# Kernel tuning notes

Measured on AMD Instinct MI355X. Metric: run time of the kernel, lower is better.

Reference implementation:

```python
import jax, jax.numpy as jnp
import numpy as np

N_NODES = 100000
N_EDGES = 1600000
IN_SIZE, HID_SIZE, OUT_SIZE = 128, 64, 64


def _glorot(key, shape):
    lim = float(np.sqrt(6.0 / (shape[0] + shape[1])))
    return jax.random.uniform(key, shape, jnp.float32, -lim, lim)


def setup_inputs() -> dict:
    key = jax.random.key(0)
    ks = jax.random.split(key, 6)
    features = jax.random.normal(ks[0], (N_NODES, IN_SIZE), jnp.float32)
    src = jax.random.randint(ks[1], (N_EDGES,), 0, N_NODES)
    dst = jax.random.randint(ks[2], (N_EDGES,), 0, N_NODES)
    return {
        "features": features,
        "W0": _glorot(ks[3], (IN_SIZE, HID_SIZE)),
        "b0": jnp.zeros((HID_SIZE,), jnp.float32),
        "W1": _glorot(ks[4], (HID_SIZE, HID_SIZE)),
        "b1": jnp.zeros((HID_SIZE,), jnp.float32),
        "W2": _glorot(ks[5], (HID_SIZE, OUT_SIZE)),
        "b2": jnp.zeros((OUT_SIZE,), jnp.float32),
        "src": src,
        "dst": dst,
    }


def reference(features, W0, b0, W1, b1, W2, b2, src, dst):
    # DGL GraphConv with norm='both': h' = relu(D_in^{-1/2} A D_out^{-1/2} h W + b)
    # Dropout layers are identity in eval mode (deterministic baseline).
    N = features.shape[0]
    ones = jnp.ones(src.shape, features.dtype)
    deg_out = jax.ops.segment_sum(ones, src, num_segments=N)
    deg_in = jax.ops.segment_sum(ones, dst, num_segments=N)
    norm_src = jnp.where(deg_out > 0, deg_out, 1.0) ** -0.5  # [N]
    norm_dst = jnp.where(deg_in > 0, deg_in, 1.0) ** -0.5    # [N]

    def layer(h, W, b):
        h = h * norm_src[:, None]          # source-side degree norm
        m = (h @ W)[src]                   # project first (in >= out), then gather [E, d_out]
        agg = jax.ops.segment_sum(m, dst, num_segments=N)  # scatter-add to destinations
        return jax.nn.relu(agg * norm_dst[:, None] + b)

    h = layer(features, W0, b0)
    h = layer(h, W1, b1)
    return layer(h, W2, b2)
```

## Files before the change

kernel.cpp:

```cpp
#include <hip/hip_runtime.h>
#include <hip/hip_bf16.h>

typedef __hip_bfloat16 bf16;
typedef __attribute__((ext_vector_type(8))) short bf16x8;
typedef __attribute__((ext_vector_type(8))) unsigned short u16x8;
typedef __attribute__((ext_vector_type(4))) float f32x4;
typedef __attribute__((ext_vector_type(4))) int i32x4;
typedef __attribute__((ext_vector_type(4))) short s16x4;

__device__ __forceinline__ float b2f(unsigned short u) {
  return __uint_as_float(((unsigned)u) << 16);
}
__device__ __forceinline__ unsigned short f2b(float x) {
  bf16 h = __float2bfloat16(x);
  return *reinterpret_cast<unsigned short*>(&h);
}

__global__ void k_passA(const int* __restrict__ src, const int* __restrict__ dst, int E,
                        int nbuck, int M, int* __restrict__ counts,
                        const unsigned short* __restrict__ raw, int* __restrict__ flag) {
  if (blockIdx.x == 256) {
    __shared__ int sbad, snz;
    const int t = threadIdx.x;
    if (t == 0) { sbad = 0; snz = 0; }
    __syncthreads();
    const unsigned short u = raw[t];
    const float a = fabsf(b2f(u));
    if (!(a < 100.f)) atomicAdd(&sbad, 1);
    if (((t & 1) == 0) && u != 0) atomicAdd(&snz, 1);
    __syncthreads();
    if (t == 0) flag[0] = (sbad == 0 && snz > 0) ? 1 : 0;
    return;
  }
  extern __shared__ int lh[];
  int* lh1 = lh;
  int* lh2 = lh + nbuck;
  const int t = threadIdx.x;
  for (int k = t; k < 2 * nbuck; k += 256) lh[k] = 0;
  __syncthreads();
  const int chunk = (E + 255) / 256;
  const int s = blockIdx.x * chunk;
  const int e = min(E, s + chunk);
  for (int i = s + t; i < e; i += 256) {
    atomicAdd(&lh1[dst[i] >> 8], 1);
    atomicAdd(&lh2[src[i] >> 8], 1);
  }
  __syncthreads();
  for (int k = t; k < nbuck; k += 256) {
    counts[k * 256 + blockIdx.x] = lh1[k];
    counts[M + k * 256 + blockIdx.x] = lh2[k];
  }
}

__global__ void k_scan1(const int* __restrict__ a, int M2, int* __restrict__ bsums) {
  __shared__ int sdata[256];
  int i = blockIdx.x * 256 + threadIdx.x;
  int v = (i < M2) ? a[i] : 0;
  sdata[threadIdx.x] = v;
  __syncthreads();
  for (int s = 128; s > 0; s >>= 1) {
    if (threadIdx.x < s) sdata[threadIdx.x] += sdata[threadIdx.x + s];
    __syncthreads();
  }
  if (threadIdx.x == 0) bsums[blockIdx.x] = sdata[0];
}

__global__ void k_scan2(int* __restrict__ bsums, int nb, int* __restrict__ rowStart,
                        int N, int E) {
  __shared__ int s[1024];
  const int t = threadIdx.x;
  const int v = (t < nb) ? bsums[t] : 0;
  s[t] = v;
  __syncthreads();
  for (int off = 1; off < 1024; off <<= 1) {
    int u = (t >= off) ? s[t - off] : 0;
    __syncthreads();
    s[t] += u;
    __syncthreads();
  }
  if (t < nb) bsums[t] = s[t] - v;
  if (t == 0) rowStart[N] = E;
}

__global__ void k_scan3(int* __restrict__ a, int M2, const int* __restrict__ bsums) {
  __shared__ int sdata[256];
  int i = blockIdx.x * 256 + threadIdx.x;
  int v = (i < M2) ? a[i] : 0;
  sdata[threadIdx.x] = v;
  __syncthreads();
  for (int off = 1; off < 256; off <<= 1) {
    int t = (threadIdx.x >= off) ? sdata[threadIdx.x - off] : 0;
    __syncthreads();
    sdata[threadIdx.x] += t;
    __syncthreads();
  }
  if (i < M2) a[i] = bsums[blockIdx.x] + sdata[threadIdx.x] - v;
}

__global__ void k_passC(const int* __restrict__ src, const int* __restrict__ dst, int E,
                        int nbuck, int M, const int* __restrict__ S,
                        int* __restrict__ tmp, unsigned char* __restrict__ tmp2) {
  extern __shared__ int cur[];
  int* cur1 = cur;
  int* cur2 = cur + nbuck;
  const int t = threadIdx.x;
  for (int k = t; k < nbuck; k += 256) {
    cur1[k] = S[k * 256 + blockIdx.x];
    cur2[k] = S[M + k * 256 + blockIdx.x];
  }
  __syncthreads();
  const int chunk = (E + 255) / 256;
  const int s = blockIdx.x * chunk;
  const int e = min(E, s + chunk);
  for (int i = s + t; i < e; i += 256) {
    const int sv = src[i];
    const int d = dst[i];
    const int pos1 = atomicAdd(&cur1[d >> 8], 1);
    tmp[pos1] = sv | ((d & 255) << 20);
    const int pos2 = atomicAdd(&cur2[sv >> 8], 1);
    tmp2[pos2 - E] = (unsigned char)(sv & 255);
  }
}

__global__ void k_passD(const int* __restrict__ tmp, const unsigned char* __restrict__ tmp2,
                        const int* __restrict__ S, int nbuck, int M, int N, int E,
                        int* __restrict__ rowStart, int* __restrict__ edgeSrc,
                        float* __restrict__ ns, float* __restrict__ nd) {
  __shared__ int h[256];
  __shared__ int ex[256];
  __shared__ int c[256];
  const int t = threadIdx.x;
  const int k = blockIdx.x;
  const int node = k * 256 + t;
  const int bs2 = S[M + k * 256] - E;
  const int be2 = (k + 1 < nbuck) ? (S[M + (k + 1) * 256] - E) : E;
  h[t] = 0;
  __syncthreads();
  for (int i = bs2 + t; i < be2; i += 256) atomicAdd(&h[tmp2[i]], 1);
  __syncthreads();
  if (node < N) {
    int dov = h[t];
    if (dov <= 0) dov = 1;
    ns[node] = rsqrtf((float)dov);
  }
  __syncthreads();
  const int bs = S[k * 256];
  const int be = (k + 1 < nbuck) ? S[(k + 1) * 256] : E;
  h[t] = 0;
  __syncthreads();
  for (int i = bs + t; i < be; i += 256) atomicAdd(&h[tmp[i] >> 20], 1);
  __syncthreads();
  const int cnt = h[t];
  ex[t] = cnt;
  __syncthreads();
  for (int off = 1; off < 256; off <<= 1) {
    int u = (t >= off) ? ex[t - off] : 0;
    __syncthreads();
    ex[t] += u;
    __syncthreads();
  }
  const int excl = ex[t] - cnt;
  if (node < N) {
    rowStart[node] = bs + excl;
    nd[node] = rsqrtf((float)(cnt > 0 ? cnt : 1));
  }
  c[t] = bs + excl;
  __syncthreads();
  for (int i = bs + t; i < be; i += 256) {
    const int v = tmp[i];
    const int pos = atomicAdd(&c[v >> 20], 1);
    edgeSrc[pos] = v & 0xFFFFF;
  }
}

template <int K, bool FIRST, bool SCALE>
__global__ void k_gemm(const void* __restrict__ hin, const void* __restrict__ Wv,
                       const int* __restrict__ flag, const float* __restrict__ norm_src,
                       int N, unsigned short* __restrict__ out) {
  const bool isb = (*flag != 0);
  const int lane = threadIdx.x & 63;
  const int quad = lane >> 4;
  const int l16 = lane & 15;
  constexpr int KT = K / 32;

  bf16x8 Bf[KT][4];
  {
    const unsigned short* Wus = (const unsigned short*)Wv;
    const float* Wf = (const float*)Wv;
#pragma unroll
    for (int kt = 0; kt < KT; ++kt)
#pragma unroll
      for (int nt = 0; nt < 4; ++nt)
#pragma unroll
        for (int j = 0; j < 8; ++j) {
          const int k = kt * 32 + quad * 8 + j;
          const int n = nt * 16 + l16;
          const float w = isb ? b2f(Wus[k * 64 + n]) : Wf[k * 64 + n];
          Bf[kt][nt][j] = (short)f2b(w);
        }
  }
  const int wid = (blockIdx.x * blockDim.x + threadIdx.x) >> 6;
  const int nw = (gridDim.x * blockDim.x) >> 6;
  const int G = (N + 15) >> 4;
  for (int g = wid; g < G; g += nw) {
    int rowA = (g << 4) + l16;
    if (rowA >= N) rowA = N - 1;
    f32x4 acc[4] = {{0.f, 0.f, 0.f, 0.f}, {0.f, 0.f, 0.f, 0.f},
                    {0.f, 0.f, 0.f, 0.f}, {0.f, 0.f, 0.f, 0.f}};
#pragma unroll
    for (int kt = 0; kt < KT; ++kt) {
      const int koff = kt * 32 + quad * 8;
      bf16x8 Af;
      if (FIRST && !isb) {
        const float* hp = (const float*)hin + (size_t)rowA * K + koff;
        const float4 u0 = *(const float4*)hp;
        const float4 u1 = *(const float4*)(hp + 4);
        Af[0] = (short)f2b(u0.x); Af[1] = (short)f2b(u0.y);
        Af[2] = (short)f2b(u0.z); Af[3] = (short)f2b(u0.w);
        Af[4] = (short)f2b(u1.x); Af[5] = (short)f2b(u1.y);
        Af[6] = (short)f2b(u1.z); Af[7] = (short)f2b(u1.w);
      } else {
        Af = *(const bf16x8*)((const unsigned short*)hin + (size_t)rowA * K + koff);
      }
      acc[0] = __builtin_amdgcn_mfma_f32_16x16x32_bf16(Af, Bf[kt][0], acc[0], 0, 0, 0);
      acc[1] = __builtin_amdgcn_mfma_f32_16x16x32_bf16(Af, Bf[kt][1], acc[1], 0, 0, 0);
      acc[2] = __builtin_amdgcn_mfma_f32_16x16x32_bf16(Af, Bf[kt][2], acc[2], 0, 0, 0);
      acc[3] = __builtin_amdgcn_mfma_f32_16x16x32_bf16(Af, Bf[kt][3], acc[3], 0, 0, 0);
    }
    const int rowD = (g << 4) + quad * 4;
#pragma unroll
    for (int r = 0; r < 4; ++r) {
      if (rowD + r < N) {
        const float f = SCALE ? norm_src[rowD + r] : 1.0f;
        const size_t o = (size_t)(rowD + r) * 64 + l16;
#pragma unroll
        for (int nt = 0; nt < 4; ++nt)
          out[o + nt * 16] = f2b(SCALE ? acc[nt][r] * f : acc[nt][r]);
      }
    }
  }
}

__device__ __forceinline__ void agg_chunk_compute(unsigned trbase, int cb32, int lo,
                                                  unsigned span, int quad, f32x4* acc) {
  const int posbase = cb32 + (quad << 2);
  const unsigned u0 = (unsigned)(posbase - lo);
  bf16x8 Af;
#pragma unroll
  for (int j = 0; j < 8; ++j) {
    const unsigned off = (j < 4) ? (unsigned)j : (unsigned)(12 + j);
    Af[j] = ((u0 + off) < span) ? (short)0x3F80 : (short)0;
  }
  s16x4 t0[4], t1[4];
#pragma unroll
  for (int nt = 0; nt < 4; ++nt) {
    const unsigned a = trbase + (unsigned)(nt * 1024);
    asm volatile("ds_read_b64_tr_b16 %0, %1" : "=v"(t0[nt]) : "v"(a) : "memory");
    asm volatile("ds_read_b64_tr_b16 %0, %1 offset:512" : "=v"(t1[nt]) : "v"(a) : "memory");
  }
  asm volatile("s_waitcnt lgkmcnt(0)" ::: "memory");
  __builtin_amdgcn_sched_barrier(0);
#pragma unroll
  for (int nt = 0; nt < 4; ++nt) {
    bf16x8 Bf;
    Bf[0] = t0[nt][0]; Bf[1] = t0[nt][1]; Bf[2] = t0[nt][2]; Bf[3] = t0[nt][3];
    Bf[4] = t1[nt][0]; Bf[5] = t1[nt][1]; Bf[6] = t1[nt][2]; Bf[7] = t1[nt][3];
    acc[nt] = __builtin_amdgcn_mfma_f32_16x16x32_bf16(Af, Bf, acc[nt], 0, 0, 0);
  }
}

template <bool LAST>
__global__ void __launch_bounds__(256) k_aggregate(
    const unsigned short* __restrict__ proj,
    const int* __restrict__ edgeSrc, const int* __restrict__ rowStart,
    const float* __restrict__ norm_dst, const float* __restrict__ norm_src,
    const void* __restrict__ bias, const int* __restrict__ flag,
    int N, int E, void* __restrict__ outp) {
  __shared__ unsigned short lds[4][2048];
  const bool isb = (*flag != 0);
  const int tid = threadIdx.x;
  const int w = tid >> 6;
  const int lane = tid & 63;
  const int l16 = lane & 15;
  const int quad = lane >> 4;
  const int e32 = lane & 31;
  const int p = lane >> 5;

  const int wid = blockIdx.x * 4 + w;
  const int g0 = wid * 8;

  float bcol[4];
#pragma unroll
  for (int nt = 0; nt < 4; ++nt) {
    const int col = nt * 16 + l16;
    bcol[nt] = isb ? b2f(((const unsigned short*)bias)[col]) : ((const float*)bias)[col];
  }

  const int cb = rowStart[min(g0, N)];
  const int ce = rowStart[min(g0 + 8, N)];
  const int L = ce - cb;
  const int nch = (L + 31) >> 5;

  const int rsi = min(g0 + min(l16, 8), N);
  const int rsj = min(g0 + min(l16 + 1, 8), N);
  const int lo = rowStart[rsi];
  const unsigned span = (unsigned)(rowStart[rsj] - lo);

  int idxc[6];
#pragma unroll
  for (int t = 0; t < 6; ++t) {
    const int pos = min(cb + t * 32 + e32, E - 1);
    idxc[t] = edgeSrc[pos];
  }

  unsigned short* myl = &lds[w][0];
  unsigned wofs[4];
#pragma unroll
  for (int q = 0; q < 4; ++q) {
    const int n0 = p * 32 + q * 8;
    wofs[q] = (unsigned)((n0 >> 4) * 512 + e32 * 16 + (n0 & 15));
  }
  const unsigned trbase = (unsigned)(uintptr_t)myl + (unsigned)lane * 8u;

  f32x4 acc[4] = {{0.f, 0.f, 0.f, 0.f}, {0.f, 0.f, 0.f, 0.f},
                  {0.f, 0.f, 0.f, 0.f}, {0.f, 0.f, 0.f, 0.f}};

  i32x4 gb[2][4];
#define AGG_ISSUE(t, b)                                                         \
  {                                                                             \
    const unsigned short* rp = proj + (size_t)idxc[t] * 64 + p * 32;            \
    gb[b][0] = *(const i32x4*)(rp);                                             \
    gb[b][1] = *(const i32x4*)(rp + 8);                                         \
    gb[b][2] = *(const i32x4*)(rp + 16);                                        \
    gb[b][3] = *(const i32x4*)(rp + 24);                                        \
  }
  if (0 < nch) AGG_ISSUE(0, 0);
  if (1 < nch) AGG_ISSUE(1, 1);

#pragma unroll
  for (int tt = 0; tt < 6; ++tt) {
    if (tt < nch) {
#pragma unroll
      for (int q = 0; q < 4; ++q) *(i32x4*)(myl + wofs[q]) = gb[tt & 1][q];
      if (tt + 2 < 6 && tt + 2 < nch) AGG_ISSUE(tt + 2, tt & 1);
      asm volatile("s_waitcnt lgkmcnt(0)" ::: "memory");
      agg_chunk_compute(trbase, cb + tt * 32, lo, span, quad, acc);
    }
  }
  for (int t = 6; t < nch; ++t) {
    const int pos = min(cb + t * 32 + e32, E - 1);
    const int idx = edgeSrc[pos];
    const unsigned short* rp = proj + (size_t)idx * 64 + p * 32;
    i32x4 g4[4];
    g4[0] = *(const i32x4*)(rp);
    g4[1] = *(const i32x4*)(rp + 8);
    g4[2] = *(const i32x4*)(rp + 16);
    g4[3] = *(const i32x4*)(rp + 24);
#pragma unroll
    for (int q = 0; q < 4; ++q) *(i32x4*)(myl + wofs[q]) = g4[q];
    asm volatile("s_waitcnt lgkmcnt(0)" ::: "memory");
    agg_chunk_compute(trbase, cb + t * 32, lo, span, quad, acc);
  }
#undef AGG_ISSUE

#pragma unroll
  for (int reg = 0; reg < 4; ++reg) {
    const int row = quad * 4 + reg;
    const int node = g0 + row;
    if (row < 8 && node < N) {
      const float nd = norm_dst[node];
      const float esc = LAST ? 1.f : norm_src[node];
#pragma unroll
      for (int nt = 0; nt < 4; ++nt) {
        float x = fmaxf(fmaf(acc[nt][reg], nd, bcol[nt]), 0.f);
        if (!LAST) x *= esc;
        const size_t o = (size_t)node * 64 + nt * 16 + l16;
        if (LAST && !isb)
          ((float*)outp)[o] = x;
        else
          ((unsigned short*)outp)[o] = f2b(x);
      }
    }
  }
}

extern "C" void kernel_launch(void* const* d_in, const int* in_sizes, int n_in,
                              void* d_out, int out_size, void* d_ws, size_t ws_size,
                              hipStream_t stream) {
  const void* features = d_in[0];
  const void* W0 = d_in[1];
  const void* b0 = d_in[2];
  const void* W1 = d_in[3];
  const void* b1 = d_in[4];
  const void* W2 = d_in[5];
  const void* b2 = d_in[6];
  const int* src = (const int*)d_in[7];
  const int* dst = (const int*)d_in[8];
  const int N = in_sizes[0] / 128;
  const int E = in_sizes[7];
  const int NBUCK = (N + 255) >> 8;
  const int M = NBUCK * 256;
  const int M2 = 2 * M;

  char* w = (char*)d_ws;
  size_t off = 0;
  auto alloc = [&](size_t bytes) {
    void* p = w + off;
    off = (off + bytes + 255) & ~(size_t)255;
    return p;
  };
  int* flag = (int*)alloc(4);
  int* rowStart = (int*)alloc((size_t)(N + 1) * 4);
  int* counts = (int*)alloc((size_t)M2 * 4);
  int* bsums = (int*)alloc(1024 * 4);
  float* norm_src = (float*)alloc((size_t)N * 4);
  float* norm_dst = (float*)alloc((size_t)N * 4);
  int* tmp = (int*)alloc((size_t)E * 4);
  unsigned char* tmp2 = (unsigned char*)alloc((size_t)E);
  int* edgeSrc = (int*)alloc((size_t)E * 4);
  unsigned short* projA = (unsigned short*)alloc((size_t)N * 64 * 2);
  unsigned short* hB = (unsigned short*)d_out;

  const size_t lds_nb = (size_t)NBUCK * 2 * 4;
  const int GB = ((N + 15) / 16 + 3) / 4;

  k_passA<<<257, 256, lds_nb, stream>>>(src, dst, E, NBUCK, M, counts,
                                        (const unsigned short*)features, flag);
  const int NB2 = (M2 + 255) / 256;
  k_scan1<<<NB2, 256, 0, stream>>>(counts, M2, bsums);
  k_scan2<<<1, 1024, 0, stream>>>(bsums, NB2, rowStart, N, E);
  k_scan3<<<NB2, 256, 0, stream>>>(counts, M2, bsums);
  k_passC<<<256, 256, lds_nb, stream>>>(src, dst, E, NBUCK, M, counts, tmp, tmp2);
  k_passD<<<NBUCK, 256, 0, stream>>>(tmp, tmp2, counts, NBUCK, M, N, E,
                                     rowStart, edgeSrc, norm_src, norm_dst);

  const int AB = (((N + 7) / 8) + 3) / 4;
  k_gemm<128, true, true><<<GB, 256, 0, stream>>>(features, W0, flag, norm_src, N, projA);
  k_aggregate<false><<<AB, 256, 0, stream>>>(projA, edgeSrc, rowStart, norm_dst, norm_src, b0, flag, N, E, hB);
  k_gemm<64, false, false><<<GB, 256, 0, stream>>>(hB, W1, flag, nullptr, N, projA);
  k_aggregate<false><<<AB, 256, 0, stream>>>(projA, edgeSrc, rowStart, norm_dst, norm_src, b1, flag, N, E, hB);
  k_gemm<64, false, false><<<GB, 256, 0, stream>>>(hB, W2, flag, nullptr, N, projA);
  k_aggregate<true><<<AB, 256, 0, stream>>>(projA, edgeSrc, rowStart, norm_dst, norm_src, b2, flag, N, E, d_out);
}
```

Measured before the change: 339.3 us.

## Stage GEMM weights in LDS and coalesce output stores via LDS transpose

Each block now loads the weight matrix once into padded shared memory, converting to bf16 cooperatively, instead of every wave gathering its own register copy with scalar strided loads. The GEMM output is staged through a per-wave LDS tile so that each row is written with 16-byte vector stores rather than scattered 2-byte stores. The grid becomes a fixed 1024 blocks that loop over row groups. This trades added LDS traffic and a block barrier for fewer redundant global weight loads and better-coalesced writes.

```diff
diff --git a/kernel.cpp b/kernel.cpp
--- a/kernel.cpp
+++ b/kernel.cpp
@@ -174,34 +174,51 @@
 }
 
 template <int K, bool FIRST, bool SCALE>
-__global__ void k_gemm(const void* __restrict__ hin, const void* __restrict__ Wv,
-                       const int* __restrict__ flag, const float* __restrict__ norm_src,
-                       int N, unsigned short* __restrict__ out) {
+__global__ void __launch_bounds__(256) k_gemm(
+    const void* __restrict__ hin, const void* __restrict__ Wv,
+    const int* __restrict__ flag, const float* __restrict__ norm_src,
+    int N, unsigned short* __restrict__ out) {
+  constexpr int ST = K + 8;
+  constexpr int CST = 72;
+  __shared__ unsigned short Wl[64 * ST];
+  __shared__ unsigned short Cl[4][16 * CST];
   const bool isb = (*flag != 0);
-  const int lane = threadIdx.x & 63;
-  const int quad = lane >> 4;
-  const int l16 = lane & 15;
-  constexpr int KT = K / 32;
-
-  bf16x8 Bf[KT][4];
+  const int tid = threadIdx.x;
+
   {
     const unsigned short* Wus = (const unsigned short*)Wv;
     const float* Wf = (const float*)Wv;
-#pragma unroll
-    for (int kt = 0; kt < KT; ++kt)
-#pragma unroll
-      for (int nt = 0; nt < 4; ++nt)
-#pragma unroll
-        for (int j = 0; j < 8; ++j) {
-          const int k = kt * 32 + quad * 8 + j;
-          const int n = nt * 16 + l16;
-          const float w = isb ? b2f(Wus[k * 64 + n]) : Wf[k * 64 + n];
-          Bf[kt][nt][j] = (short)f2b(w);
-        }
-  }
-  const int wid = (blockIdx.x * blockDim.x + threadIdx.x) >> 6;
-  const int nw = (gridDim.x * blockDim.x) >> 6;
+    for (int i0 = tid * 8; i0 < K * 64; i0 += 2048) {
+      const int k = i0 >> 6;
+      const int n0 = i0 & 63;
+      unsigned short v[8];
+      if (isb) {
+        const u16x8 u = *(const u16x8*)(Wus + i0);
+#pragma unroll
+        for (int j = 0; j < 8; ++j) v[j] = u[j];
+      } else {
+        const float4 f0 = *(const float4*)(Wf + i0);
+        const float4 f1 = *(const float4*)(Wf + i0 + 4);
+        v[0] = f2b(f0.x); v[1] = f2b(f0.y); v[2] = f2b(f0.z); v[3] = f2b(f0.w);
+        v[4] = f2b(f1.x); v[5] = f2b(f1.y); v[6] = f2b(f1.z); v[7] = f2b(f1.w);
+      }
+#pragma unroll
+      for (int j = 0; j < 8; ++j) Wl[(n0 + j) * ST + k] = v[j];
+    }
+  }
+  __syncthreads();
+
+  const int lane = tid & 63;
+  const int quad = lane >> 4;
+  const int l16 = lane & 15;
+  const int w = tid >> 6;
+  unsigned short* myC = &Cl[w][0];
+
+  const int wid = blockIdx.x * 4 + w;
+  const int nw = gridDim.x * 4;
   const int G = (N + 15) >> 4;
+  constexpr int KT = K / 32;
+
   for (int g = wid; g < G; g += nw) {
     int rowA = (g << 4) + l16;
     if (rowA >= N) rowA = N - 1;
@@ -222,21 +239,29 @@
       } else {
         Af = *(const bf16x8*)((const unsigned short*)hin + (size_t)rowA * K + koff);
       }
-      acc[0] = __builtin_amdgcn_mfma_f32_16x16x32_bf16(Af, Bf[kt][0], acc[0], 0, 0, 0);
-      acc[1] = __builtin_amdgcn_mfma_f32_16x16x32_bf16(Af, Bf[kt][1], acc[1], 0, 0, 0);
-      acc[2] = __builtin_amdgcn_mfma_f32_16x16x32_bf16(Af, Bf[kt][2], acc[2], 0, 0, 0);
-      acc[3] = __builtin_amdgcn_mfma_f32_16x16x32_bf16(Af, Bf[kt][3], acc[3], 0, 0, 0);
-    }
-    const int rowD = (g << 4) + quad * 4;
+#pragma unroll
+      for (int nt = 0; nt < 4; ++nt) {
+        const bf16x8 Bf = *(const bf16x8*)&Wl[(nt * 16 + l16) * ST + koff];
+        acc[nt] = __builtin_amdgcn_mfma_f32_16x16x32_bf16(Af, Bf, acc[nt], 0, 0, 0);
+      }
+    }
+    const int rowD = quad * 4;
 #pragma unroll
     for (int r = 0; r < 4; ++r) {
-      if (rowD + r < N) {
-        const float f = SCALE ? norm_src[rowD + r] : 1.0f;
-        const size_t o = (size_t)(rowD + r) * 64 + l16;
-#pragma unroll
-        for (int nt = 0; nt < 4; ++nt)
-          out[o + nt * 16] = f2b(SCALE ? acc[nt][r] * f : acc[nt][r]);
-      }
+      const int nodeW = (g << 4) + rowD + r;
+      const float f = (SCALE && nodeW < N) ? norm_src[nodeW] : 1.0f;
+#pragma unroll
+      for (int nt = 0; nt < 4; ++nt)
+        myC[(rowD + r) * CST + nt * 16 + l16] = f2b(SCALE ? acc[nt][r] * f : acc[nt][r]);
+    }
+    const int row2 = lane >> 2;
+    const int c0 = (lane & 3) * 16;
+    const int node = (g << 4) + row2;
+    if (node < N) {
+      const u16x8 v0 = *(const u16x8*)&myC[row2 * CST + c0];
+      const u16x8 v1 = *(const u16x8*)&myC[row2 * CST + c0 + 8];
+      *(u16x8*)(out + (size_t)node * 64 + c0) = v0;
+      *(u16x8*)(out + (size_t)node * 64 + c0 + 8) = v1;
     }
   }
 }
@@ -422,7 +447,7 @@
   unsigned short* hB = (unsigned short*)d_out;
 
   const size_t lds_nb = (size_t)NBUCK * 2 * 4;
-  const int GB = ((N + 15) / 16 + 3) / 4;
+  const int GB = 1024;
 
   k_passA<<<257, 256, lds_nb, stream>>>(src, dst, E, NBUCK, M, counts,
                                         (const unsigned short*)features, flag);
```

New measurement: 312.0 us. 1.09x faster.
